# Optimization experiments

Hardware: AMD Instinct MI355X
Metric: run time of the kernel (lower is better)

Reference implementation:

```python
import jax, jax.numpy as jnp
import numpy as np

B, N, D, NS, H, ITERS = 16, 2048, 128, 8, 128, 3
EPS = 1e-8


def _ln(x, g, b):
    m = jnp.mean(x, -1, keepdims=True)
    v = jnp.mean((x - m) ** 2, -1, keepdims=True)
    return (x - m) * jax.lax.rsqrt(v + 1e-5) * g + b


def _gru(x, h, Wih, Whh, bih, bhh):
    # PyTorch GRUCell math
    gi = x @ Wih.T + bih
    gh = h @ Whh.T + bhh
    ir, iz, inn = jnp.split(gi, 3, -1)
    hr, hz, hn = jnp.split(gh, 3, -1)
    r = jax.nn.sigmoid(ir + hr)
    z = jax.nn.sigmoid(iz + hz)
    n = jnp.tanh(inn + r * hn)
    return (1.0 - z) * n + z * h


def setup_inputs() -> dict:
    key = jax.random.key(0)
    ks = jax.random.split(key, 16)

    def lin(k, out_d, in_d):
        lim = 1.0 / np.sqrt(in_d)
        return jax.random.uniform(k, (out_d, in_d), jnp.float32, -lim, lim)

    return {
        "inputs": jax.random.normal(ks[0], (B, N, D), jnp.float32),
        "init_noise": jax.random.normal(ks[1], (B, NS, 2 * D), jnp.float32),
        "slots_mu": jax.random.normal(ks[2], (1, 1, 2 * D), jnp.float32),
        "slots_logsigma": jax.random.normal(ks[3], (1, 1, 2 * D), jnp.float32) * 0.08,  # ~xavier scale
        "Wq": lin(ks[4], D, D),
        "Wk": lin(ks[5], D, D),
        "gru_Wih": lin(ks[6], 3 * D, D),
        "gru_Whh": lin(ks[7], 3 * D, D),
        "gru_bih": jnp.zeros((3 * D,), jnp.float32),
        "gru_bhh": jnp.zeros((3 * D,), jnp.float32),
        "mlp_mu_W1": lin(ks[8], H, D),
        "mlp_mu_b1": jnp.zeros((H,), jnp.float32),
        "mlp_mu_W2": lin(ks[9], D, H),
        "mlp_mu_b2": jnp.zeros((D,), jnp.float32),
        "ln_in_g": jnp.ones((D,), jnp.float32),
        "ln_in_b": jnp.zeros((D,), jnp.float32),
        "ln_slots_g": jnp.ones((2 * D,), jnp.float32),
        "ln_slots_b": jnp.zeros((2 * D,), jnp.float32),
        "ln_mu_g": jnp.ones((D,), jnp.float32),
        "ln_mu_b": jnp.zeros((D,), jnp.float32),
        "mlp_out_W1": lin(ks[10], 2 * H, 2 * D),
        "mlp_out_b1": jnp.zeros((2 * H,), jnp.float32),
        "mlp_out_W2": lin(ks[11], D, 2 * H),
        "mlp_out_b2": jnp.zeros((D,), jnp.float32),
    }


def _forward(inputs, init_noise, slots_mu, slots_logsigma, Wq, Wk,
             gru_Wih, gru_Whh, gru_bih, gru_bhh,
             mlp_mu_W1, mlp_mu_b1, mlp_mu_W2, mlp_mu_b2,
             ln_in_g, ln_in_b, ln_slots_g, ln_slots_b, ln_mu_g, ln_mu_b,
             mlp_out_W1, mlp_out_b1, mlp_out_W2, mlp_out_b2):
    x = _ln(inputs, ln_in_g, ln_in_b)                      # (B,N,D)
    k = x @ Wk.T
    v = k                                                  # original uses to_k for both k and v
    slots = slots_mu + jnp.exp(slots_logsigma) * init_noise  # (B,NS,2D)
    pi_cl = jnp.full((B, NS, 1), 1.0 / NS, inputs.dtype)

    def step(slots, pi_cl):
        s = _ln(slots, ln_slots_g, ln_slots_b)
        mu_s, ls_s = jnp.split(s, 2, -1)                   # (B,NS,D) each
        q_mu = mu_s @ Wq.T
        q_ls = ls_s @ Wq.T
        inv_var = jnp.exp(-2.0 * q_ls)                     # 1 / exp(q_logsigma)^2
        diff = k[:, None, :, :] - q_mu[:, :, None, :]      # (B,NS,N,D)
        dots = jnp.einsum('bind,bid->bin', diff * diff, inv_var)
        dots_exp = (jnp.exp(-dots) + EPS) * pi_cl          # (B,NS,N)
        gammas = dots_exp / dots_exp.sum(1, keepdims=True)
        attn = gammas / gammas.sum(-1, keepdims=True)
        upd = jnp.einsum('bjd,bij->bid', v, attn)          # (B,NS,D)
        upd = _gru(upd.reshape(-1, D), mu_s.reshape(-1, D),
                   gru_Wih, gru_Whh, gru_bih, gru_bhh).reshape(B, NS, D)
        h = _ln(upd, ln_mu_g, ln_mu_b)
        upd = upd + (jax.nn.relu(h @ mlp_mu_W1.T + mlp_mu_b1) @ mlp_mu_W2.T + mlp_mu_b2)
        diff2 = v[:, None, :, :] - upd[:, :, None, :]      # (B,NS,N,D)
        upd_ls = 0.5 * jnp.log(jnp.einsum('bind,bin->bid', diff2 * diff2 + EPS, attn))
        slots_new = jnp.concatenate([upd, upd_ls], -1)
        pi_new = gammas.sum(-1, keepdims=True)
        pi_new = pi_new / pi_new.shape[2]                  # shape[2]==1: faithful no-op from original
        return slots_new, pi_new

    for _ in range(ITERS):
        slots, pi_cl = step(slots, pi_cl)
    slots, pi_cl = step(jax.lax.stop_gradient(slots), pi_cl)
    h = jax.nn.relu(slots @ mlp_out_W1.T + mlp_out_b1)
    return h @ mlp_out_W2.T + mlp_out_b2                   # (B,NS,D)


def reference(inputs, init_noise, slots_mu, slots_logsigma, Wq, Wk,
              gru_Wih, gru_Whh, gru_bih, gru_bhh,
              mlp_mu_W1, mlp_mu_b1, mlp_mu_W2, mlp_mu_b2,
              ln_in_g, ln_in_b, ln_slots_g, ln_slots_b, ln_mu_g, ln_mu_b,
              mlp_out_W1, mlp_out_b1, mlp_out_W2, mlp_out_b2):
    return _forward(inputs, init_noise, slots_mu, slots_logsigma, Wq, Wk,
                    gru_Wih, gru_Whh, gru_bih, gru_bhh,
                    mlp_mu_W1, mlp_mu_b1, mlp_mu_W2, mlp_mu_b2,
                    ln_in_g, ln_in_b, ln_slots_g, ln_slots_b, ln_mu_g, ln_mu_b,
                    mlp_out_W1, mlp_out_b1, mlp_out_W2, mlp_out_b2)
```

## Files before the change

kernel.cpp:

```cpp
#include <hip/hip_runtime.h>

#define EPS_ 1e-8f

constexpr int OFF_K     = 0;
constexpr int OFF_WQT   = 4194304;
constexpr int OFF_WKT   = OFF_WQT  + 16384;
constexpr int OFF_WIHT  = OFF_WKT  + 16384;
constexpr int OFF_WHHT  = OFF_WIHT + 49152;
constexpr int OFF_WM1T  = OFF_WHHT + 49152;
constexpr int OFF_WM2T  = OFF_WM1T + 16384;
constexpr int OFF_WO1T  = OFF_WM2T + 16384;
constexpr int OFF_WO2T  = OFF_WO1T + 65536;
constexpr int OFF_SLOTS = OFF_WO2T + 32768;
constexpr int OFF_PI    = OFF_SLOTS+ 32768;
constexpr int OFF_MUS   = OFF_PI   + 128;
constexpr int OFF_WA    = OFF_MUS  + 16384;
constexpr int OFF_WB    = OFF_WA   + 16384;
constexpr int OFF_UN    = OFF_WB   + 16384;
constexpr int OFF_S2    = OFF_UN   + 524288;
constexpr int OFF_DEN   = OFF_S2   + 524288;
constexpr int OFF_CZ    = OFF_DEN  + 4096;

__global__ __launch_bounds__(256) void init_kernel(
    const float* __restrict__ Wq,  const float* __restrict__ Wk,
    const float* __restrict__ Wih, const float* __restrict__ Whh,
    const float* __restrict__ Wm1, const float* __restrict__ Wm2,
    const float* __restrict__ Wo1, const float* __restrict__ Wo2,
    const float* __restrict__ smu, const float* __restrict__ sls,
    const float* __restrict__ noise, float* __restrict__ ws) {
  int idx = blockIdx.x * 256 + threadIdx.x;
  if (idx < 16384) { int j = idx >> 7, d = idx & 127; ws[OFF_WQT + d*128 + j] = Wq[idx]; return; }
  idx -= 16384;
  if (idx < 16384) { int j = idx >> 7, d = idx & 127; ws[OFF_WKT + d*128 + j] = Wk[idx]; return; }
  idx -= 16384;
  if (idx < 49152) { int j = idx >> 7, d = idx & 127; ws[OFF_WIHT + d*384 + j] = Wih[idx]; return; }
  idx -= 49152;
  if (idx < 49152) { int j = idx >> 7, d = idx & 127; ws[OFF_WHHT + d*384 + j] = Whh[idx]; return; }
  idx -= 49152;
  if (idx < 16384) { int j = idx >> 7, d = idx & 127; ws[OFF_WM1T + d*128 + j] = Wm1[idx]; return; }
  idx -= 16384;
  if (idx < 16384) { int j = idx >> 7, d = idx & 127; ws[OFF_WM2T + d*128 + j] = Wm2[idx]; return; }
  idx -= 16384;
  if (idx < 65536) { int j = idx >> 8, d = idx & 255; ws[OFF_WO1T + d*256 + j] = Wo1[idx]; return; }
  idx -= 65536;
  if (idx < 32768) { int j = idx >> 8, m = idx & 255; ws[OFF_WO2T + m*128 + j] = Wo2[idx]; return; }
  idx -= 32768;
  if (idx < 32768) { int c = idx & 255; ws[OFF_SLOTS + idx] = smu[c] + expf(sls[c]) * noise[idx]; return; }
  idx -= 32768;
  if (idx < 128) { ws[OFF_PI + idx] = 0.125f; }
}

__global__ __launch_bounds__(256) void k_kernel(
    const float* __restrict__ xin, const float* __restrict__ g, const float* __restrict__ bb,
    const float* __restrict__ WkT, float* __restrict__ kout) {
  __shared__ float xs[16][129];
  __shared__ float2 red[16][16];
  __shared__ float mrow[16], srow[16];
  int t = threadIdx.x;
  long long base = (long long)blockIdx.x * 16 * 128;
  const float4* in4 = (const float4*)(xin + base);
  for (int f = t; f < 512; f += 256) {
    float4 v = in4[f];
    int r = f >> 5, c = (f & 31) * 4;
    xs[r][c] = v.x; xs[r][c + 1] = v.y; xs[r][c + 2] = v.z; xs[r][c + 3] = v.w;
  }
  __syncthreads();
  {
    int row = t >> 4, l = t & 15;
    float s = 0.f, ss = 0.f;
    #pragma unroll
    for (int dd = 0; dd < 128; dd += 16) { float v = xs[row][dd + l]; s += v; ss = fmaf(v, v, ss); }
    red[row][l] = make_float2(s, ss);
  }
  __syncthreads();
  if (t < 16) {
    float s = 0.f, ss = 0.f;
    #pragma unroll
    for (int l = 0; l < 16; ++l) { float2 p = red[t][l]; s += p.x; ss += p.y; }
    float m = s * (1.0f / 128.0f);
    float var = ss * (1.0f / 128.0f) - m * m;
    mrow[t] = m;
    srow[t] = rsqrtf(var + 1e-5f);
  }
  __syncthreads();
  for (int f = t; f < 2048; f += 256) {
    int row = f >> 7, d = f & 127;
    xs[row][d] = (xs[row][d] - mrow[row]) * srow[row] * g[d] + bb[d];
  }
  __syncthreads();
  int j4 = t & 31, rg = t >> 5;
  int r0 = rg * 2;
  float a00 = 0, a01 = 0, a02 = 0, a03 = 0;
  float a10 = 0, a11 = 0, a12 = 0, a13 = 0;
  #pragma unroll 4
  for (int d = 0; d < 128; ++d) {
    float4 wv = *(const float4*)(WkT + d * 128 + j4 * 4);
    float x0 = xs[r0][d], x1 = xs[r0 + 1][d];
    a00 = fmaf(x0, wv.x, a00); a01 = fmaf(x0, wv.y, a01);
    a02 = fmaf(x0, wv.z, a02); a03 = fmaf(x0, wv.w, a03);
    a10 = fmaf(x1, wv.x, a10); a11 = fmaf(x1, wv.y, a11);
    a12 = fmaf(x1, wv.z, a12); a13 = fmaf(x1, wv.w, a13);
  }
  float* o0 = kout + base + (long long)r0 * 128 + j4 * 4;
  *(float4*)o0         = make_float4(a00, a01, a02, a03);
  *(float4*)(o0 + 128) = make_float4(a10, a11, a12, a13);
}

__global__ __launch_bounds__(256) void s1_kernel(
    const float* __restrict__ slots, const float* __restrict__ g, const float* __restrict__ bb,
    const float* __restrict__ WqT, float* __restrict__ mus,
    float* __restrict__ wA, float* __restrict__ wB, float* __restrict__ cz) {
  __shared__ float sl[256];
  __shared__ float2 wr[4];
  __shared__ float qs_l[128], ivs_l[128];
  __shared__ float wrC[4];
  int t = threadIdx.x, bi = blockIdx.x;
  float v = slots[bi * 256 + t];
  float s = v, ss = v * v;
  #pragma unroll
  for (int o = 32; o > 0; o >>= 1) { s += __shfl_down(s, o); ss += __shfl_down(ss, o); }
  if ((t & 63) == 0) wr[t >> 6] = make_float2(s, ss);
  __syncthreads();
  float fs  = wr[0].x + wr[1].x + wr[2].x + wr[3].x;
  float fss = wr[0].y + wr[1].y + wr[2].y + wr[3].y;
  float m   = fs * (1.0f/256.0f);
  float var = fss * (1.0f/256.0f) - m * m;
  float isr = rsqrtf(var + 1e-5f);
  float sn  = (v - m) * isr * g[t] + bb[t];
  sl[t] = sn;
  __syncthreads();
  if (t < 128) {
    float acc = 0.f;
    #pragma unroll 4
    for (int d = 0; d < 128; ++d) acc = fmaf(sl[d], WqT[d * 128 + t], acc);
    qs_l[t] = acc;
    mus[bi * 128 + t] = sn;
  } else {
    int jj = t - 128;
    float acc = 0.f;
    #pragma unroll 4
    for (int d = 0; d < 128; ++d) acc = fmaf(sl[128 + d], WqT[d * 128 + jj], acc);
    ivs_l[jj] = expf(-2.0f * acc);
  }
  __syncthreads();
  float cp = 0.f;
  if (t < 128) {
    float iv = ivs_l[t], q = qs_l[t];
    wA[bi * 128 + t] = iv;
    wB[bi * 128 + t] = -2.0f * q * iv;
    cp = q * q * iv;
  }
  #pragma unroll
  for (int o = 32; o > 0; o >>= 1) cp += __shfl_down(cp, o);
  if ((t & 63) == 0) wrC[t >> 6] = cp;
  __syncthreads();
  if (t == 0) cz[bi] = wrC[0] + wrC[1];
}

__global__ __launch_bounds__(512) void s2_kernel(
    const float* __restrict__ kmat, const float* __restrict__ wA,
    const float* __restrict__ wB,  const float* __restrict__ cz,
    const float* __restrict__ pi,
    float* __restrict__ wun, float* __restrict__ ws2, float* __restrict__ wden) {
  __shared__ float pdots[16][64][8];
  __shared__ float es[64][9];
  __shared__ float recip[64];
  __shared__ float gT[8][72];
  __shared__ float pd[8][8];
  __shared__ float pisl[8], czl[8];
  int t = threadIdx.x;
  int chunk = blockIdx.x, b = blockIdx.y;
  if (t < 8) { pisl[t] = pi[b * 8 + t]; czl[t] = cz[b * 8 + t]; }
  {
    int w = t & 15, nt = t >> 4;
    int n0 = nt * 2;
    const float4* kr4 = (const float4*)(kmat + (long long)(b * 2048 + chunk * 64) * 128);
    const float4* wa4 = (const float4*)(wA + b * 1024);
    const float4* wb4 = (const float4*)(wB + b * 1024);
    float acc0[8] = {0,0,0,0,0,0,0,0};
    float acc1[8] = {0,0,0,0,0,0,0,0};
    #pragma unroll
    for (int i = 0; i < 2; ++i) {
      int gg = i * 16 + w;
      float4 k0 = kr4[n0 * 32 + gg];
      float4 k1 = kr4[(n0 + 1) * 32 + gg];
      float x0 = k0.x * k0.x, y0 = k0.y * k0.y, z0 = k0.z * k0.z, w0 = k0.w * k0.w;
      float x1 = k1.x * k1.x, y1 = k1.y * k1.y, z1 = k1.z * k1.z, w1 = k1.w * k1.w;
      #pragma unroll
      for (int s = 0; s < 8; ++s) {
        float4 a4 = wa4[s * 32 + gg];
        float4 b4 = wb4[s * 32 + gg];
        float c0 = acc0[s], c1 = acc1[s];
        c0 = fmaf(x0, a4.x, c0); c0 = fmaf(k0.x, b4.x, c0);
        c0 = fmaf(y0, a4.y, c0); c0 = fmaf(k0.y, b4.y, c0);
        c0 = fmaf(z0, a4.z, c0); c0 = fmaf(k0.z, b4.z, c0);
        c0 = fmaf(w0, a4.w, c0); c0 = fmaf(k0.w, b4.w, c0);
        c1 = fmaf(x1, a4.x, c1); c1 = fmaf(k1.x, b4.x, c1);
        c1 = fmaf(y1, a4.y, c1); c1 = fmaf(k1.y, b4.y, c1);
        c1 = fmaf(z1, a4.z, c1); c1 = fmaf(k1.z, b4.z, c1);
        c1 = fmaf(w1, a4.w, c1); c1 = fmaf(k1.w, b4.w, c1);
        acc0[s] = c0; acc1[s] = c1;
      }
    }
    *(float4*)&pdots[w][n0][0]     = make_float4(acc0[0], acc0[1], acc0[2], acc0[3]);
    *(float4*)&pdots[w][n0][4]     = make_float4(acc0[4], acc0[5], acc0[6], acc0[7]);
    *(float4*)&pdots[w][n0 + 1][0] = make_float4(acc1[0], acc1[1], acc1[2], acc1[3]);
    *(float4*)&pdots[w][n0 + 1][4] = make_float4(acc1[4], acc1[5], acc1[6], acc1[7]);
  }
  __syncthreads();
  float e;
  {
    int n2 = t >> 3, s = t & 7;
    float dots = czl[s];
    #pragma unroll
    for (int w = 0; w < 16; ++w) dots += pdots[w][n2][s];
    e = (expf(-dots) + EPS_) * pisl[s];
    es[n2][s] = e;
  }
  __syncthreads();
  if (t < 64) {
    float ssum = 0.f;
    #pragma unroll
    for (int s = 0; s < 8; ++s) ssum += es[t][s];
    recip[t] = 1.0f / ssum;
  }
  __syncthreads();
  {
    int n2 = t >> 3, s = t & 7;
    float gam = e * recip[n2];
    gT[s][n2] = gam;
    float p = gam;
    p += __shfl_down(p, 8); p += __shfl_down(p, 16); p += __shfl_down(p, 32);
    if ((t & 63) < 8) pd[t >> 6][t & 7] = p;
  }
  __syncthreads();
  if (t < 8) {
    float sden = 0.f;
    #pragma unroll
    for (int w = 0; w < 8; ++w) sden += pd[w][t];
    wden[(b * 32 + chunk) * 8 + t] = sden;
  }
  {
    int d = t & 127, sh = t >> 7;
    int s0 = sh * 2, s1 = s0 + 1;
    const float* kcol = kmat + (long long)(b * 2048 + chunk * 64) * 128 + d;
    float u0 = 0.f, u1 = 0.f, q0 = 0.f, q1 = 0.f;
    #pragma unroll 2
    for (int n3 = 0; n3 < 64; n3 += 4) {
      float4 ga = *(const float4*)&gT[s0][n3];
      float4 gb = *(const float4*)&gT[s1][n3];
      float k0 = kcol[(n3 + 0) * 128];
      float k1 = kcol[(n3 + 1) * 128];
      float k2 = kcol[(n3 + 2) * 128];
      float k3 = kcol[(n3 + 3) * 128];
      float k0s = k0 * k0, k1s = k1 * k1, k2s = k2 * k2, k3s = k3 * k3;
      u0 = fmaf(ga.x, k0, u0); q0 = fmaf(ga.x, k0s, q0);
      u1 = fmaf(gb.x, k0, u1); q1 = fmaf(gb.x, k0s, q1);
      u0 = fmaf(ga.y, k1, u0); q0 = fmaf(ga.y, k1s, q0);
      u1 = fmaf(gb.y, k1, u1); q1 = fmaf(gb.y, k1s, q1);
      u0 = fmaf(ga.z, k2, u0); q0 = fmaf(ga.z, k2s, q0);
      u1 = fmaf(gb.z, k2, u1); q1 = fmaf(gb.z, k2s, q1);
      u0 = fmaf(ga.w, k3, u0); q0 = fmaf(ga.w, k3s, q0);
      u1 = fmaf(gb.w, k3, u1); q1 = fmaf(gb.w, k3s, q1);
    }
    int pb = ((b * 32 + chunk) * 8) * 128 + d;
    wun[pb + s0 * 128] = u0; wun[pb + s1 * 128] = u1;
    ws2[pb + s0 * 128] = q0; ws2[pb + s1 * 128] = q1;
  }
}

__global__ __launch_bounds__(512) void s3_kernel(
    const float* __restrict__ wun, const float* __restrict__ ws2, const float* __restrict__ wden,
    const float* __restrict__ WihT, const float* __restrict__ WhhT,
    const float* __restrict__ bih,  const float* __restrict__ bhh,
    const float* __restrict__ Wm1T, const float* __restrict__ bm1,
    const float* __restrict__ Wm2T, const float* __restrict__ bm2,
    const float* __restrict__ gmu,  const float* __restrict__ bmu,
    float* __restrict__ slots, float* __restrict__ pi,
    int do_s1,
    const float* __restrict__ gs, const float* __restrict__ bs,
    const float* __restrict__ WqT,
    float* __restrict__ mus, float* __restrict__ wAo, float* __restrict__ wBo,
    float* __restrict__ czo,
    const float* __restrict__ Wo1T, const float* __restrict__ bo1,
    const float* __restrict__ Wo2T, const float* __restrict__ bo2,
    float* __restrict__ out) {
  int t = threadIdx.x, bi = blockIdx.x;
  int d = t & 127, q = t >> 7;
  int b = bi >> 3, i = bi & 7;
  __shared__ float redU[4][128], redS[4][128];
  __shared__ float dred[32];
  __shared__ float xs[128], hs[128];
  __shared__ float gacc[4][6][128];
  __shared__ float ga[6][128];
  __shared__ float grus[128], hl[128], m1s[128];
  __shared__ float macc[4][128];
  __shared__ float2 wr2[2];
  __shared__ float uarr[256];
  float unp = 0.f, s2p = 0.f;
  #pragma unroll
  for (int c = q * 8; c < q * 8 + 8; ++c) {
    int po = ((b * 32 + c) * 8 + i) * 128 + d;
    unp += wun[po]; s2p += ws2[po];
  }
  redU[q][d] = unp; redS[q][d] = s2p;
  if (t < 32) dred[t] = wden[(b * 32 + t) * 8 + i];
  if (q == 1) hs[d] = mus[bi * 128 + d];
  __syncthreads();
  float den = 0.f;
  #pragma unroll
  for (int c = 0; c < 32; ++c) den += dred[c];
  float un  = redU[0][d] + redU[1][d] + redU[2][d] + redU[3][d];
  float s2v = redS[0][d] + redS[1][d] + redS[2][d] + redS[3][d];
  if (q == 0) xs[d] = un / den;
  __syncthreads();
  {
    float a0 = 0, a1 = 0, a2 = 0, a3 = 0, a4 = 0, a5 = 0;
    #pragma unroll 4
    for (int dd = q * 32; dd < q * 32 + 32; ++dd) {
      float xv = xs[dd], hv = hs[dd];
      const float* wi = &WihT[dd * 384 + d];
      const float* wh = &WhhT[dd * 384 + d];
      a0 = fmaf(xv, wi[0],   a0);
      a1 = fmaf(xv, wi[128], a1);
      a2 = fmaf(xv, wi[256], a2);
      a3 = fmaf(hv, wh[0],   a3);
      a4 = fmaf(hv, wh[128], a4);
      a5 = fmaf(hv, wh[256], a5);
    }
    gacc[q][0][d] = a0; gacc[q][1][d] = a1; gacc[q][2][d] = a2;
    gacc[q][3][d] = a3; gacc[q][4][d] = a4; gacc[q][5][d] = a5;
  }
  __syncthreads();
  for (int f = t; f < 768; f += 512) {
    int j = f >> 7, dd = f & 127;
    ga[j][dd] = gacc[0][j][dd] + gacc[1][j][dd] + gacc[2][j][dd] + gacc[3][j][dd];
  }
  __syncthreads();
  float gru = 0.f;
  if (q == 0) {
    float ir = ga[0][d] + bih[d], iz = ga[1][d] + bih[128 + d], inn = ga[2][d] + bih[256 + d];
    float hr = ga[3][d] + bhh[d], hz = ga[4][d] + bhh[128 + d], hn  = ga[5][d] + bhh[256 + d];
    float r  = 1.0f / (1.0f + expf(-(ir + hr)));
    float z  = 1.0f / (1.0f + expf(-(iz + hz)));
    float nn = tanhf(inn + r * hn);
    gru = (1.0f - z) * nn + z * hs[d];
    grus[d] = gru;
    float s = gru, ssq = gru * gru;
    #pragma unroll
    for (int o = 32; o > 0; o >>= 1) { s += __shfl_down(s, o); ssq += __shfl_down(ssq, o); }
    if ((d & 63) == 0) wr2[d >> 6] = make_float2(s, ssq);
  }
  __syncthreads();
  if (q == 0) {
    float fs = wr2[0].x + wr2[1].x, fss = wr2[0].y + wr2[1].y;
    float mean = fs * (1.0f/128.0f);
    float var  = fss * (1.0f/128.0f) - mean * mean;
    hl[d] = (gru - mean) * rsqrtf(var + 1e-5f) * gmu[d] + bmu[d];
  }
  __syncthreads();
  {
    float m1p = 0.f;
    #pragma unroll 4
    for (int dd = q * 32; dd < q * 32 + 32; ++dd)
      m1p = fmaf(hl[dd], Wm1T[dd * 128 + d], m1p);
    macc[q][d] = m1p;
  }
  __syncthreads();
  if (q == 0) m1s[d] = fmaxf(macc[0][d] + macc[1][d] + macc[2][d] + macc[3][d] + bm1[d], 0.f);
  __syncthreads();
  {
    float m2p = 0.f;
    #pragma unroll 4
    for (int dd = q * 32; dd < q * 32 + 32; ++dd)
      m2p = fmaf(m1s[dd], Wm2T[dd * 128 + d], m2p);
    macc[q][d] = m2p;
  }
  __syncthreads();
  if (q == 0) {
    float u = grus[d] + macc[0][d] + macc[1][d] + macc[2][d] + macc[3][d] + bm2[d];
    float val = (s2v - 2.0f * u * un + u * u * den) / den;
    float ls = 0.5f * logf(fmaxf(val, 0.0f) + EPS_);
    slots[bi * 256 + d]       = u;
    slots[bi * 256 + 128 + d] = ls;
    uarr[d] = u; uarr[128 + d] = ls;
    if (d == 0) pi[bi] = den;
  }
  __syncthreads();
  if (do_s1) {
    __shared__ float2 wr4[4];
    __shared__ float sln[256];
    __shared__ float qacc[2][2][128];
    __shared__ float qs_l[128], ivs_l[128];
    __shared__ float wrC[8];
    if (t < 256) {
      float v2 = uarr[t];
      float s = v2, ssq = v2 * v2;
      #pragma unroll
      for (int o = 32; o > 0; o >>= 1) { s += __shfl_down(s, o); ssq += __shfl_down(ssq, o); }
      if ((t & 63) == 0) wr4[t >> 6] = make_float2(s, ssq);
    }
    __syncthreads();
    if (t < 256) {
      float fs  = wr4[0].x + wr4[1].x + wr4[2].x + wr4[3].x;
      float fss = wr4[0].y + wr4[1].y + wr4[2].y + wr4[3].y;
      float m   = fs * (1.0f/256.0f);
      float var = fss * (1.0f/256.0f) - m * m;
      sln[t] = (uarr[t] - m) * rsqrtf(var + 1e-5f) * gs[t] + bs[t];
    }
    __syncthreads();
    {
      int h2 = t >> 8, qq = (t >> 7) & 1, d2 = t & 127;
      const float* src = sln + h2 * 128;
      float acc = 0.f;
      #pragma unroll 4
      for (int dd = qq * 64; dd < qq * 64 + 64; ++dd)
        acc = fmaf(src[dd], WqT[dd * 128 + d2], acc);
      qacc[h2][qq][d2] = acc;
    }
    __syncthreads();
    if (t < 128) {
      qs_l[t] = qacc[0][0][t] + qacc[0][1][t];
      mus[bi * 128 + t] = sln[t];
    } else if (t < 256) {
      int dd2 = t - 128;
      ivs_l[dd2] = expf(-2.0f * (qacc[1][0][dd2] + qacc[1][1][dd2]));
    }
    __syncthreads();
    float cp = 0.f;
    if (t < 128) {
      float iv = ivs_l[t], qv = qs_l[t];
      wAo[bi * 128 + t] = iv;
      wBo[bi * 128 + t] = -2.0f * qv * iv;
      cp = qv * qv * iv;
    }
    #pragma unroll
    for (int o = 32; o > 0; o >>= 1) cp += __shfl_down(cp, o);
    if ((t & 63) == 0) wrC[t >> 6] = cp;
    __syncthreads();
    if (t == 0) czo[bi] = wrC[0] + wrC[1];
  } else {
    __shared__ float oacc[2][256];
    __shared__ float hh[256];
    {
      int o = t & 255, qq = t >> 8;
      float acc = 0.f;
      #pragma unroll 4
      for (int dd = qq * 128; dd < qq * 128 + 128; ++dd)
        acc = fmaf(uarr[dd], Wo1T[dd * 256 + o], acc);
      oacc[qq][o] = acc;
    }
    __syncthreads();
    if (t < 256) hh[t] = fmaxf(oacc[0][t] + oacc[1][t] + bo1[t], 0.f);
    __syncthreads();
    {
      int o2 = t & 127, q4 = t >> 7;
      float acc2 = 0.f;
      #pragma unroll 4
      for (int dd = q4 * 64; dd < q4 * 64 + 64; ++dd)
        acc2 = fmaf(hh[dd], Wo2T[dd * 128 + o2], acc2);
      macc[q4][o2] = acc2;
    }
    __syncthreads();
    if (t < 128) out[bi * 128 + t] = macc[0][t] + macc[1][t] + macc[2][t] + macc[3][t] + bo2[t];
  }
}

extern "C" void kernel_launch(void* const* d_in, const int* in_sizes, int n_in,
                              void* d_out, int out_size, void* d_ws, size_t ws_size,
                              hipStream_t stream) {
  const float* inputs = (const float*)d_in[0];
  const float* noise  = (const float*)d_in[1];
  const float* smu    = (const float*)d_in[2];
  const float* sls    = (const float*)d_in[3];
  const float* Wq     = (const float*)d_in[4];
  const float* Wk     = (const float*)d_in[5];
  const float* Wih    = (const float*)d_in[6];
  const float* Whh    = (const float*)d_in[7];
  const float* bih    = (const float*)d_in[8];
  const float* bhh    = (const float*)d_in[9];
  const float* Wm1    = (const float*)d_in[10];
  const float* bm1    = (const float*)d_in[11];
  const float* Wm2    = (const float*)d_in[12];
  const float* bm2    = (const float*)d_in[13];
  const float* gin    = (const float*)d_in[14];
  const float* bin    = (const float*)d_in[15];
  const float* gsl    = (const float*)d_in[16];
  const float* bsl    = (const float*)d_in[17];
  const float* gmu    = (const float*)d_in[18];
  const float* bmu    = (const float*)d_in[19];
  const float* Wo1    = (const float*)d_in[20];
  const float* bo1    = (const float*)d_in[21];
  const float* Wo2    = (const float*)d_in[22];
  const float* bo2    = (const float*)d_in[23];

  float* ws    = (float*)d_ws;
  float* kbuf  = ws + OFF_K;
  float* WqT   = ws + OFF_WQT;
  float* WkT   = ws + OFF_WKT;
  float* WihT  = ws + OFF_WIHT;
  float* WhhT  = ws + OFF_WHHT;
  float* Wm1T  = ws + OFF_WM1T;
  float* Wm2T  = ws + OFF_WM2T;
  float* Wo1T  = ws + OFF_WO1T;
  float* Wo2T  = ws + OFF_WO2T;
  float* slots = ws + OFF_SLOTS;
  float* pibuf = ws + OFF_PI;
  float* mus   = ws + OFF_MUS;
  float* wA    = ws + OFF_WA;
  float* wB    = ws + OFF_WB;
  float* wun   = ws + OFF_UN;
  float* ws2   = ws + OFF_S2;
  float* wden  = ws + OFF_DEN;
  float* czb   = ws + OFF_CZ;

  hipLaunchKernelGGL(init_kernel, dim3(1153), dim3(256), 0, stream,
                     Wq, Wk, Wih, Whh, Wm1, Wm2, Wo1, Wo2, smu, sls, noise, ws);
  hipLaunchKernelGGL(k_kernel, dim3(2048), dim3(256), 0, stream,
                     inputs, gin, bin, WkT, kbuf);
  hipLaunchKernelGGL(s1_kernel, dim3(128), dim3(256), 0, stream,
                     slots, gsl, bsl, WqT, mus, wA, wB, czb);
  for (int s = 0; s < 4; ++s) {
    hipLaunchKernelGGL(s2_kernel, dim3(32, 16), dim3(512), 0, stream,
                       kbuf, wA, wB, czb, pibuf, wun, ws2, wden);
    hipLaunchKernelGGL(s3_kernel, dim3(128), dim3(512), 0, stream,
                       wun, ws2, wden, WihT, WhhT, bih, bhh,
                       Wm1T, bm1, Wm2T, bm2, gmu, bmu, slots, pibuf,
                       (s < 3) ? 1 : 0, gsl, bsl, WqT, mus, wA, wB, czb,
                       Wo1T, bo1, Wo2T, bo2, (float*)d_out);
  }
}
```

Baseline: 178.2 us.

## Retile key projection kernel to 64 rows per block with transposed LDS

The LayerNorm plus Wk projection kernel now processes 64 rows per block instead of 16, with each thread computing an 8x4 output tile instead of 2x4. Input rows are loaded into registers, normalized, and stored transposed in LDS so the inner loop reads activations as float4. This raises arithmetic intensity per weight load and cuts the number of global reads of WkT by 4x. The cost is higher register pressure and fewer blocks (512), which may reduce occupancy.

```diff
diff --git a/kernel.cpp b/kernel.cpp
--- a/kernel.cpp
+++ b/kernel.cpp
@@ -53,57 +53,75 @@
 __global__ __launch_bounds__(256) void k_kernel(
     const float* __restrict__ xin, const float* __restrict__ g, const float* __restrict__ bb,
     const float* __restrict__ WkT, float* __restrict__ kout) {
-  __shared__ float xs[16][129];
-  __shared__ float2 red[16][16];
-  __shared__ float mrow[16], srow[16];
+  __shared__ float xsT[128][72];
+  __shared__ float2 red2[64][4];
+  __shared__ float mrow[64], srow[64];
   int t = threadIdx.x;
-  long long base = (long long)blockIdx.x * 16 * 128;
-  const float4* in4 = (const float4*)(xin + base);
-  for (int f = t; f < 512; f += 256) {
-    float4 v = in4[f];
-    int r = f >> 5, c = (f & 31) * 4;
-    xs[r][c] = v.x; xs[r][c + 1] = v.y; xs[r][c + 2] = v.z; xs[r][c + 3] = v.w;
-  }
-  __syncthreads();
-  {
-    int row = t >> 4, l = t & 15;
+  long long base = (long long)blockIdx.x * 64 * 128;
+  int r = t >> 2, q = t & 3;
+  float vals[32];
+  {
+    const float4* src = (const float4*)(xin + base + r * 128 + q * 32);
+    #pragma unroll
+    for (int i = 0; i < 8; ++i) *(float4*)&vals[i * 4] = src[i];
+  }
+  {
     float s = 0.f, ss = 0.f;
     #pragma unroll
-    for (int dd = 0; dd < 128; dd += 16) { float v = xs[row][dd + l]; s += v; ss = fmaf(v, v, ss); }
-    red[row][l] = make_float2(s, ss);
-  }
-  __syncthreads();
-  if (t < 16) {
+    for (int i = 0; i < 32; ++i) { float v = vals[i]; s += v; ss = fmaf(v, v, ss); }
+    red2[r][q] = make_float2(s, ss);
+  }
+  __syncthreads();
+  if (t < 64) {
     float s = 0.f, ss = 0.f;
     #pragma unroll
-    for (int l = 0; l < 16; ++l) { float2 p = red[t][l]; s += p.x; ss += p.y; }
+    for (int c = 0; c < 4; ++c) { float2 p = red2[t][c]; s += p.x; ss += p.y; }
     float m = s * (1.0f / 128.0f);
     float var = ss * (1.0f / 128.0f) - m * m;
-    mrow[t] = m;
-    srow[t] = rsqrtf(var + 1e-5f);
-  }
-  __syncthreads();
-  for (int f = t; f < 2048; f += 256) {
-    int row = f >> 7, d = f & 127;
-    xs[row][d] = (xs[row][d] - mrow[row]) * srow[row] * g[d] + bb[d];
+    mrow[t] = m; srow[t] = rsqrtf(var + 1e-5f);
+  }
+  __syncthreads();
+  {
+    float m = mrow[r], is = srow[r];
+    #pragma unroll 8
+    for (int u = 0; u < 32; ++u) {
+      int d = q * 32 + u;
+      xsT[d][r] = (vals[u] - m) * is * g[d] + bb[d];
+    }
   }
   __syncthreads();
   int j4 = t & 31, rg = t >> 5;
-  int r0 = rg * 2;
-  float a00 = 0, a01 = 0, a02 = 0, a03 = 0;
-  float a10 = 0, a11 = 0, a12 = 0, a13 = 0;
-  #pragma unroll 4
+  int r0 = rg * 8;
+  float a0[8], a1[8], a2[8], a3[8];
+  #pragma unroll
+  for (int i = 0; i < 8; ++i) { a0[i] = 0.f; a1[i] = 0.f; a2[i] = 0.f; a3[i] = 0.f; }
+  #pragma unroll 2
   for (int d = 0; d < 128; ++d) {
     float4 wv = *(const float4*)(WkT + d * 128 + j4 * 4);
-    float x0 = xs[r0][d], x1 = xs[r0 + 1][d];
-    a00 = fmaf(x0, wv.x, a00); a01 = fmaf(x0, wv.y, a01);
-    a02 = fmaf(x0, wv.z, a02); a03 = fmaf(x0, wv.w, a03);
-    a10 = fmaf(x1, wv.x, a10); a11 = fmaf(x1, wv.y, a11);
-    a12 = fmaf(x1, wv.z, a12); a13 = fmaf(x1, wv.w, a13);
-  }
-  float* o0 = kout + base + (long long)r0 * 128 + j4 * 4;
-  *(float4*)o0         = make_float4(a00, a01, a02, a03);
-  *(float4*)(o0 + 128) = make_float4(a10, a11, a12, a13);
+    float4 x0 = *(const float4*)&xsT[d][r0];
+    float4 x1 = *(const float4*)&xsT[d][r0 + 4];
+    a0[0] = fmaf(x0.x, wv.x, a0[0]); a1[0] = fmaf(x0.x, wv.y, a1[0]);
+    a2[0] = fmaf(x0.x, wv.z, a2[0]); a3[0] = fmaf(x0.x, wv.w, a3[0]);
+    a0[1] = fmaf(x0.y, wv.x, a0[1]); a1[1] = fmaf(x0.y, wv.y, a1[1]);
+    a2[1] = fmaf(x0.y, wv.z, a2[1]); a3[1] = fmaf(x0.y, wv.w, a3[1]);
+    a0[2] = fmaf(x0.z, wv.x, a0[2]); a1[2] = fmaf(x0.z, wv.y, a1[2]);
+    a2[2] = fmaf(x0.z, wv.z, a2[2]); a3[2] = fmaf(x0.z, wv.w, a3[2]);
+    a0[3] = fmaf(x0.w, wv.x, a0[3]); a1[3] = fmaf(x0.w, wv.y, a1[3]);
+    a2[3] = fmaf(x0.w, wv.z, a2[3]); a3[3] = fmaf(x0.w, wv.w, a3[3]);
+    a0[4] = fmaf(x1.x, wv.x, a0[4]); a1[4] = fmaf(x1.x, wv.y, a1[4]);
+    a2[4] = fmaf(x1.x, wv.z, a2[4]); a3[4] = fmaf(x1.x, wv.w, a3[4]);
+    a0[5] = fmaf(x1.y, wv.x, a0[5]); a1[5] = fmaf(x1.y, wv.y, a1[5]);
+    a2[5] = fmaf(x1.y, wv.z, a2[5]); a3[5] = fmaf(x1.y, wv.w, a3[5]);
+    a0[6] = fmaf(x1.z, wv.x, a0[6]); a1[6] = fmaf(x1.z, wv.y, a1[6]);
+    a2[6] = fmaf(x1.z, wv.z, a2[6]); a3[6] = fmaf(x1.z, wv.w, a3[6]);
+    a0[7] = fmaf(x1.w, wv.x, a0[7]); a1[7] = fmaf(x1.w, wv.y, a1[7]);
+    a2[7] = fmaf(x1.w, wv.z, a2[7]); a3[7] = fmaf(x1.w, wv.w, a3[7]);
+  }
+  #pragma unroll
+  for (int i = 0; i < 8; ++i) {
+    float* o = kout + base + (long long)(r0 + i) * 128 + j4 * 4;
+    *(float4*)o = make_float4(a0[i], a1[i], a2[i], a3[i]);
+  }
 }
 
 __global__ __launch_bounds__(256) void s1_kernel(
@@ -516,7 +534,7 @@
 
   hipLaunchKernelGGL(init_kernel, dim3(1153), dim3(256), 0, stream,
                      Wq, Wk, Wih, Whh, Wm1, Wm2, Wo1, Wo2, smu, sls, noise, ws);
-  hipLaunchKernelGGL(k_kernel, dim3(2048), dim3(256), 0, stream,
+  hipLaunchKernelGGL(k_kernel, dim3(512), dim3(256), 0, stream,
                      inputs, gin, bin, WkT, kbuf);
   hipLaunchKernelGGL(s1_kernel, dim3(128), dim3(256), 0, stream,
                      slots, gsl, bsl, WqT, mus, wA, wB, czb);
```

New measurement: 176.2 us. No clear change (-1.1%).
